# Kernel tuning notes

Hardware: AMD Instinct MI355X
Metric: run time of the kernel (lower is better)

The kernel has to match this reference:

```python
import jax, jax.numpy as jnp
import numpy as np

NB_OBJECTS = 3
DIM_BODY = 10
DIM_OBJECT = 15
DIM_OBJ_FEAT = NB_OBJECTS + DIM_OBJECT  # 18
DIM_PHI_IN = 54
HID = 256
DIM_PHI_OUT = 256
DIM_RHO_OUT = 1
B = 65536

# (o1, o2) object pair and (j, k) predicate indices, as in the torch code
PAIRS = [((0, 1), (3, 5)), ((0, 2), (4, 7)), ((1, 2), (6, 8))]


def setup_inputs() -> dict:
    key = jax.random.key(0)
    ks = jax.random.split(key, 24)
    inp = {
        "obs": jax.random.normal(ks[0], (B, 55), dtype=jnp.float32),
        "ag": jax.random.uniform(ks[1], (B, 9), dtype=jnp.float32),
        "g": jax.random.uniform(ks[2], (B, 9), dtype=jnp.float32),
        "anchor_g": jax.random.uniform(ks[3], (B, 9), dtype=jnp.float32),
        "act": jax.random.normal(ks[4], (B, 4), dtype=jnp.float32),
    }
    s = 0.05
    # PhiCriticDeepSet: two independent 2-layer MLPs (streams 1 and 2)
    inp["w1"] = jax.random.normal(ks[5], (DIM_PHI_IN, HID), dtype=jnp.float32) * s
    inp["b1"] = jnp.zeros((HID,), dtype=jnp.float32)
    inp["w2"] = jax.random.normal(ks[6], (HID, DIM_PHI_OUT), dtype=jnp.float32) * s
    inp["b2"] = jnp.zeros((DIM_PHI_OUT,), dtype=jnp.float32)
    inp["w3"] = jax.random.normal(ks[7], (DIM_PHI_IN, HID), dtype=jnp.float32) * s
    inp["b3"] = jnp.zeros((HID,), dtype=jnp.float32)
    inp["w4"] = jax.random.normal(ks[8], (HID, DIM_PHI_OUT), dtype=jnp.float32) * s
    inp["b4"] = jnp.zeros((DIM_PHI_OUT,), dtype=jnp.float32)
    # RhoCriticDeepSet: two independent 2-layer heads
    inp["w5"] = jax.random.normal(ks[9], (DIM_PHI_OUT, HID), dtype=jnp.float32) * s
    inp["b5"] = jnp.zeros((HID,), dtype=jnp.float32)
    inp["w6"] = jax.random.normal(ks[10], (HID, DIM_RHO_OUT), dtype=jnp.float32) * s
    inp["b6"] = jnp.zeros((DIM_RHO_OUT,), dtype=jnp.float32)
    inp["w7"] = jax.random.normal(ks[11], (DIM_PHI_OUT, HID), dtype=jnp.float32) * s
    inp["b7"] = jnp.zeros((HID,), dtype=jnp.float32)
    inp["w8"] = jax.random.normal(ks[12], (HID, DIM_RHO_OUT), dtype=jnp.float32) * s
    inp["b8"] = jnp.zeros((DIM_RHO_OUT,), dtype=jnp.float32)
    return inp


def _build_pair_inputs(obs, ag, g, act, anchor_g):
    """combinations_trick branch: data-dependent gather of goal bits and object pairs."""
    bs = obs.shape[0]
    obs_body = obs[:, :DIM_BODY]
    eye = jnp.eye(NB_OBJECTS, dtype=obs.dtype)
    # obs_objects: [3, B, 18] = one-hot(3) ++ object state(15)
    obs_objects = jnp.stack([
        jnp.concatenate([jnp.broadcast_to(eye[i], (bs, NB_OBJECTS)),
                         obs[:, DIM_BODY + DIM_OBJECT * i: DIM_BODY + DIM_OBJECT * (i + 1)]],
                        axis=1)
        for i in range(NB_OBJECTS)], axis=0)
    bidx = jnp.arange(bs)
    inputs = []
    for i, ((o1, o2), (j, k)) in enumerate(PAIRS):
        # selector = anchor_g @ [e_j, e_k] difference = anchor_g[:, j] - anchor_g[:, k]
        sel = (anchor_g[:, j] - anchor_g[:, k]) >= 0  # [B] bool
        # idxs_bits[i] = [i, j] where sel else [i, k]
        bit2 = jnp.where(sel, j, k)  # [B] int
        ag_pair = jnp.stack([ag[:, i], ag[bidx, bit2]], axis=1)  # [B, 2]
        g_pair = jnp.stack([g[:, i], g[bidx, bit2]], axis=1)     # [B, 2]
        # idxs_objects[i] = [o1, o2] where sel else [o2, o1]
        oi = jnp.where(sel, o1, o2)  # [B]
        oj = jnp.where(sel, o2, o1)
        obj_first = obs_objects[oi, bidx]   # [B, 18] gather along object axis
        obj_second = obs_objects[oj, bidx]  # [B, 18]
        inputs.append(jnp.concatenate(
            [ag_pair, g_pair, obs_body, obj_first, obj_second, act], axis=1))
    return jnp.stack(inputs)  # [3, B, 54]


def reference(obs, ag, g, anchor_g, act,
              w1, b1, w2, b2, w3, b3, w4, b4,
              w5, b5, w6, b6, w7, b7, w8, b8):
    inp = _build_pair_inputs(obs, ag, g, act, anchor_g)  # [3, B, 54]
    # PhiCriticDeepSet (two relu-relu streams)
    x1 = jax.nn.relu(jnp.einsum('pbi,ih->pbh', jax.nn.relu(jnp.einsum('pbd,dh->pbh', inp, w1) + b1), w2) + b2)
    x2 = jax.nn.relu(jnp.einsum('pbi,ih->pbh', jax.nn.relu(jnp.einsum('pbd,dh->pbh', inp, w3) + b3), w4) + b4)
    s1 = x1.sum(axis=0)  # [B, 256] deepset sum over pairs
    s2 = x2.sum(axis=0)
    # RhoCriticDeepSet readouts
    q1 = jax.nn.relu(s1 @ w5 + b5) @ w6 + b6  # [B, 1]
    q2 = jax.nn.relu(s2 @ w7 + b7) @ w8 + b8  # [B, 1]
    return (q1, q2)
```

## Files before the change

### kernel.cpp

```cpp
#include <hip/hip_runtime.h>
#include <hip/hip_bf16.h>

typedef unsigned short u16;
typedef unsigned int   u32;

using bf8 = __attribute__((ext_vector_type(8))) __bf16;
using f4  = __attribute__((ext_vector_type(4))) float;

__device__ __forceinline__ float b2f(u16 u) {
    union { u32 i; float f; } v; v.i = ((u32)u) << 16; return v.f;
}
__device__ __forceinline__ u16 f2b(float f) {
    union { float f; u32 i; } v; v.f = f;
    u32 x = v.i;
    x += 0x7fffu + ((x >> 16) & 1u);
    return (u16)(x >> 16);
}
__device__ __forceinline__ u32 pk2(float lo, float hi) {
    union { __hip_bfloat162 h; u32 u; } v;
    v.h = __float22bfloat162_rn(make_float2(lo, hi));
    return v.u;
}

__global__ void swz_all(const float* __restrict__ w1, const float* __restrict__ w3,
                        const float* __restrict__ w2, const float* __restrict__ w4,
                        const float* __restrict__ w5, const float* __restrict__ w7,
                        u16* __restrict__ ws) {
    __shared__ u16 slab[32 * 270];
    int b = blockIdx.x, t = threadIdx.x;
    const float* src; u16* dst; int kmax, kt;
    if      (b <  2) { src = w1; dst = ws;          kmax = 54;  kt = b;      }
    else if (b <  4) { src = w3; dst = ws + 16384;  kmax = 54;  kt = b - 2;  }
    else if (b < 12) { src = w2; dst = ws + 32768;  kmax = 256; kt = b - 4;  }
    else if (b < 20) { src = w4; dst = ws + 98304;  kmax = 256; kt = b - 12; }
    else if (b < 28) { src = w5; dst = ws + 163840; kmax = 256; kt = b - 20; }
    else             { src = w7; dst = ws + 229376; kmax = 256; kt = b - 28; }

    #pragma unroll
    for (int it = 0; it < 8; ++it) {
        int flat = it * 1024 + t * 4;
        int row = flat >> 8, col = flat & 255;
        int k = kt * 32 + row;
        float4 v = make_float4(0.f, 0.f, 0.f, 0.f);
        if (k < kmax) v = *(const float4*)(src + k * 256 + col);
        u32* sp = (u32*)&slab[row * 270 + col];
        sp[0] = pk2(v.x, v.y);
        sp[1] = pk2(v.z, v.w);
    }
    __syncthreads();

    int lane = t & 63, wave = t >> 6, lr = lane & 15, kg = lane >> 4;
    #pragma unroll
    for (int i = 0; i < 4; ++i) {
        int ct = wave * 4 + i;
        u16 v[8];
        #pragma unroll
        for (int j = 0; j < 8; ++j)
            v[j] = slab[(kg * 8 + j) * 270 + ct * 16 + lr];
        uint4 o;
        o.x = (u32)v[0] | ((u32)v[1] << 16);
        o.y = (u32)v[2] | ((u32)v[3] << 16);
        o.z = (u32)v[4] | ((u32)v[5] << 16);
        o.w = (u32)v[6] | ((u32)v[7] << 16);
        *(uint4*)(dst + (size_t)(((kt * 16 + ct) * 64 + lane) * 8)) = o;
    }
}

#define H_OFF 6144
#define S2O   (32 * 256)
#define RH0O  (64 * 256)

__global__ __launch_bounds__(512, 4) void critic_kernel(
    const float* __restrict__ obs, const float* __restrict__ ag,
    const float* __restrict__ g,   const float* __restrict__ anchor,
    const float* __restrict__ act,
    const float* __restrict__ b1,  const float* __restrict__ b2,
    const float* __restrict__ b3,  const float* __restrict__ b4,
    const float* __restrict__ b5,  const float* __restrict__ b7,
    const float* __restrict__ w6,  const float* __restrict__ b6,
    const float* __restrict__ w8,  const float* __restrict__ b8,
    const u16* __restrict__ wsz, float* __restrict__ out, int B) {

    __shared__ u16 pool[H_OFF + 96 * 256];

    const int t    = threadIdx.x;
    const int lane = t & 63;
    const int wave = t >> 6;
    const int lr   = lane & 15;
    const int lg   = lane >> 4;
    const int wg   = blockIdx.x;
    const int swr  = (lr & 7) << 3;

    if (t < 192) {
        const int O1[3] = {0, 0, 1}, O2[3] = {1, 2, 2};
        const int JA[3] = {3, 4, 6}, KA[3] = {5, 7, 8};
        int rr = t >> 1, part = t & 1;
        int p = rr >> 5, bl = rr & 31;
        int b = wg * 32 + bl;
        int j = JA[p], k = KA[p];
        bool sel = (anchor[b * 9 + j] - anchor[b * 9 + k]) >= 0.0f;
        u16* row = &pool[rr * 64];
        const int sw = (rr & 7) << 3;
        const u16 ONE = 0x3F80;
        if (part == 0) {
            int bit2 = sel ? j : k;
            int oi = sel ? O1[p] : O2[p];
            row[0 ^ sw] = f2b(ag[b * 9 + p]);
            row[1 ^ sw] = f2b(ag[b * 9 + bit2]);
            row[2 ^ sw] = f2b(g[b * 9 + p]);
            row[3 ^ sw] = f2b(g[b * 9 + bit2]);
            for (int c = 0; c < 10; ++c) row[(4 + c) ^ sw] = f2b(obs[b * 55 + c]);
            row[14 ^ sw] = (oi == 0) ? ONE : 0;
            row[15 ^ sw] = (oi == 1) ? ONE : 0;
            row[16 ^ sw] = (oi == 2) ? ONE : 0;
            for (int c = 0; c < 15; ++c) row[(17 + c) ^ sw] = f2b(obs[b * 55 + 10 + 15 * oi + c]);
        } else {
            int oj = sel ? O2[p] : O1[p];
            row[32 ^ sw] = (oj == 0) ? ONE : 0;
            row[33 ^ sw] = (oj == 1) ? ONE : 0;
            row[34 ^ sw] = (oj == 2) ? ONE : 0;
            for (int c = 0; c < 15; ++c) row[(35 + c) ^ sw] = f2b(obs[b * 55 + 10 + 15 * oj + c]);
            for (int c = 0; c < 4; ++c)  row[(50 + c) ^ sw] = f2b(act[b * 4 + c]);
            for (int c = 54; c < 64; ++c) row[c ^ sw] = 0;
        }
    }
    __syncthreads();

    u32 s1w[2][2][2];
    u32 s2w[2][2][2];

    for (int net = 0; net < 2; ++net) {
        const u16* Wl1 = wsz + (net ? 16384 : 0);
        const u16* Wl2 = wsz + 32768 + (net ? 65536 : 0);
        const float* bl1 = net ? b3 : b1;
        const float* bl2 = net ? b4 : b2;

        f4 acc[6][2];
        #pragma unroll
        for (int rt = 0; rt < 6; ++rt)
            #pragma unroll
            for (int c = 0; c < 2; ++c) acc[rt][c] = (f4){0.f, 0.f, 0.f, 0.f};
        __builtin_amdgcn_s_setprio(1);
        #pragma unroll
        for (int kt = 0; kt < 2; ++kt) {
            bf8 wfr[2];
            #pragma unroll
            for (int c = 0; c < 2; ++c)
                wfr[c] = *(const bf8*)(Wl1 + (size_t)(((kt * 16 + wave * 2 + c) * 64 + lane) * 8));
            #pragma unroll
            for (int rt = 0; rt < 6; ++rt) {
                bf8 xfr = *(const bf8*)(&pool[(rt * 16 + lr) * 64 + ((kt * 32 + lg * 8) ^ swr)]);
                #pragma unroll
                for (int c = 0; c < 2; ++c)
                    acc[rt][c] = __builtin_amdgcn_mfma_f32_16x16x32_bf16(wfr[c], xfr, acc[rt][c], 0, 0, 0);
            }
        }
        __builtin_amdgcn_s_setprio(0);
        #pragma unroll
        for (int c = 0; c < 2; ++c) {
            float4 bv = *(const float4*)(bl1 + (wave * 2 + c) * 16 + lg * 4);
            #pragma unroll
            for (int rt = 0; rt < 6; ++rt) {
                uint2 w;
                w.x = pk2(fmaxf(acc[rt][c][0] + bv.x, 0.f), fmaxf(acc[rt][c][1] + bv.y, 0.f));
                w.y = pk2(fmaxf(acc[rt][c][2] + bv.z, 0.f), fmaxf(acc[rt][c][3] + bv.w, 0.f));
                *(uint2*)&pool[H_OFF + (rt * 16 + lr) * 256 + ((((wave * 2 + c) * 16) + lg * 4) ^ swr)] = w;
            }
        }
        __syncthreads();

        f4 acc2[6][2];
        #pragma unroll
        for (int rt = 0; rt < 6; ++rt)
            #pragma unroll
            for (int c = 0; c < 2; ++c) acc2[rt][c] = (f4){0.f, 0.f, 0.f, 0.f};
        __builtin_amdgcn_s_setprio(1);
        #pragma unroll
        for (int ks = 0; ks < 8; ++ks) {
            bf8 wfr[2];
            #pragma unroll
            for (int c = 0; c < 2; ++c)
                wfr[c] = *(const bf8*)(Wl2 + (size_t)(((ks * 16 + wave * 2 + c) * 64 + lane) * 8));
            #pragma unroll
            for (int rt = 0; rt < 6; ++rt) {
                bf8 hfr = *(const bf8*)(&pool[H_OFF + (rt * 16 + lr) * 256 + ((ks * 32 + lg * 8) ^ swr)]);
                #pragma unroll
                for (int c = 0; c < 2; ++c)
                    acc2[rt][c] = __builtin_amdgcn_mfma_f32_16x16x32_bf16(wfr[c], hfr, acc2[rt][c], 0, 0, 0);
            }
        }
        __builtin_amdgcn_s_setprio(0);
        #pragma unroll
        for (int c = 0; c < 2; ++c) {
            float4 bv = *(const float4*)(bl2 + (wave * 2 + c) * 16 + lg * 4);
            #pragma unroll
            for (int s = 0; s < 2; ++s) {
                f4 sv = (f4){0.f, 0.f, 0.f, 0.f};
                #pragma unroll
                for (int p = 0; p < 3; ++p) {
                    sv[0] += fmaxf(acc2[p * 2 + s][c][0] + bv.x, 0.f);
                    sv[1] += fmaxf(acc2[p * 2 + s][c][1] + bv.y, 0.f);
                    sv[2] += fmaxf(acc2[p * 2 + s][c][2] + bv.z, 0.f);
                    sv[3] += fmaxf(acc2[p * 2 + s][c][3] + bv.w, 0.f);
                }
                if (net == 0) {
                    s1w[s][c][0] = pk2(sv[0], sv[1]);
                    s1w[s][c][1] = pk2(sv[2], sv[3]);
                } else {
                    s2w[s][c][0] = pk2(sv[0], sv[1]);
                    s2w[s][c][1] = pk2(sv[2], sv[3]);
                }
            }
        }
        __syncthreads();
    }

    #pragma unroll
    for (int s = 0; s < 2; ++s)
        #pragma unroll
        for (int c = 0; c < 2; ++c) {
            int base = H_OFF + (s * 16 + lr) * 256 + ((((wave * 2 + c) * 16) + lg * 4) ^ swr);
            *(uint2*)&pool[base]       = *(uint2*)&s1w[s][c][0];
            *(uint2*)&pool[base + S2O] = *(uint2*)&s2w[s][c][0];
        }
    __syncthreads();

    {
        const u16* W5 = wsz + 163840;
        const u16* W7 = wsz + 229376;
        f4 racc[4][2];
        #pragma unroll
        for (int rt = 0; rt < 4; ++rt)
            #pragma unroll
            for (int c = 0; c < 2; ++c) racc[rt][c] = (f4){0.f, 0.f, 0.f, 0.f};
        __builtin_amdgcn_s_setprio(1);
        #pragma unroll
        for (int ks = 0; ks < 8; ++ks) {
            bf8 w5f[2], w7f[2];
            #pragma unroll
            for (int c = 0; c < 2; ++c) {
                size_t off = (size_t)(((ks * 16 + wave * 2 + c) * 64 + lane) * 8);
                w5f[c] = *(const bf8*)(W5 + off);
                w7f[c] = *(const bf8*)(W7 + off);
            }
            #pragma unroll
            for (int rt = 0; rt < 2; ++rt) {
                bf8 s1f = *(const bf8*)(&pool[H_OFF + (rt * 16 + lr) * 256 + ((ks * 32 + lg * 8) ^ swr)]);
                bf8 s2f = *(const bf8*)(&pool[H_OFF + S2O + (rt * 16 + lr) * 256 + ((ks * 32 + lg * 8) ^ swr)]);
                #pragma unroll
                for (int c = 0; c < 2; ++c) {
                    racc[rt][c]     = __builtin_amdgcn_mfma_f32_16x16x32_bf16(w5f[c], s1f, racc[rt][c], 0, 0, 0);
                    racc[2 + rt][c] = __builtin_amdgcn_mfma_f32_16x16x32_bf16(w7f[c], s2f, racc[2 + rt][c], 0, 0, 0);
                }
            }
        }
        __builtin_amdgcn_s_setprio(0);
        #pragma unroll
        for (int c = 0; c < 2; ++c) {
            float4 bv = *(const float4*)(b5 + (wave * 2 + c) * 16 + lg * 4);
            #pragma unroll
            for (int rt = 0; rt < 2; ++rt) {
                uint2 w;
                w.x = pk2(fmaxf(racc[rt][c][0] + bv.x, 0.f), fmaxf(racc[rt][c][1] + bv.y, 0.f));
                w.y = pk2(fmaxf(racc[rt][c][2] + bv.z, 0.f), fmaxf(racc[rt][c][3] + bv.w, 0.f));
                *(uint2*)&pool[H_OFF + RH0O + (rt * 16 + lr) * 256 + ((((wave * 2 + c) * 16) + lg * 4) ^ swr)] = w;
            }
        }
        __syncthreads();
        #pragma unroll
        for (int c = 0; c < 2; ++c) {
            float4 bv = *(const float4*)(b7 + (wave * 2 + c) * 16 + lg * 4);
            #pragma unroll
            for (int rt = 0; rt < 2; ++rt) {
                uint2 w;
                w.x = pk2(fmaxf(racc[2 + rt][c][0] + bv.x, 0.f), fmaxf(racc[2 + rt][c][1] + bv.y, 0.f));
                w.y = pk2(fmaxf(racc[2 + rt][c][2] + bv.z, 0.f), fmaxf(racc[2 + rt][c][3] + bv.w, 0.f));
                *(uint2*)&pool[H_OFF + (rt * 16 + lr) * 256 + ((((wave * 2 + c) * 16) + lg * 4) ^ swr)] = w;
            }
        }
        __syncthreads();
    }

    {
        int net = lane >> 5, r = lane & 31;
        int hoff = net ? H_OFF : H_OFF + RH0O;
        const float* wv = net ? w8 : w6;
        const int swq = (r & 7) << 3;
        float s = 0.f;
        #pragma unroll
        for (int it = 0; it < 8; ++it) {
            uint2 two = *(const uint2*)&pool[hoff + r * 256 + ((wave * 32 + it * 4) ^ swq)];
            float4 wq = *(const float4*)(wv + wave * 32 + it * 4);
            s += __uint_as_float(two.x << 16)          * wq.x;
            s += __uint_as_float(two.x & 0xffff0000u)  * wq.y;
            s += __uint_as_float(two.y << 16)          * wq.z;
            s += __uint_as_float(two.y & 0xffff0000u)  * wq.w;
        }
        ((u32*)pool)[t] = __float_as_uint(s);
    }
    __syncthreads();
    if (t < 64) {
        int net = t >> 5, r = t & 31;
        float qv = net ? b8[0] : b6[0];
        #pragma unroll
        for (int p = 0; p < 8; ++p)
            qv += __uint_as_float(((u32*)pool)[p * 64 + t]);
        out[net * B + wg * 32 + r] = qv;
    }
}

extern "C" void kernel_launch(void* const* d_in, const int* in_sizes, int n_in,
                              void* d_out, int out_size, void* d_ws, size_t ws_size,
                              hipStream_t stream) {
    const float* obs = (const float*)d_in[0];
    const float* ag  = (const float*)d_in[1];
    const float* g   = (const float*)d_in[2];
    const float* anc = (const float*)d_in[3];
    const float* act = (const float*)d_in[4];
    const float* w1  = (const float*)d_in[5];
    const float* b1  = (const float*)d_in[6];
    const float* w2  = (const float*)d_in[7];
    const float* b2  = (const float*)d_in[8];
    const float* w3  = (const float*)d_in[9];
    const float* b3  = (const float*)d_in[10];
    const float* w4  = (const float*)d_in[11];
    const float* b4  = (const float*)d_in[12];
    const float* w5  = (const float*)d_in[13];
    const float* b5  = (const float*)d_in[14];
    const float* w6  = (const float*)d_in[15];
    const float* b6  = (const float*)d_in[16];
    const float* w7  = (const float*)d_in[17];
    const float* b7  = (const float*)d_in[18];
    const float* w8  = (const float*)d_in[19];
    const float* b8  = (const float*)d_in[20];
    u16* ws    = (u16*)d_ws;
    float* out = (float*)d_out;
    int B = in_sizes[0] / 55;

    swz_all<<<36, 256, 0, stream>>>(w1, w3, w2, w4, w5, w7, ws);
    critic_kernel<<<(B + 31) / 32, 512, 0, stream>>>(obs, ag, g, anc, act,
                                                     b1, b2, b3, b4, b5, b7,
                                                     w6, b6, w8, b8, ws, out, B);
}
```

Measured before the change: 191.4 us.

## Retile waves as 2x4 grid so each wave reuses X fragments across four column tiles

Changes the 8-wave work split from each wave owning 2 output-column tiles across all 6 row tiles to a 2x4 grid. Each wave now owns 4 column tiles and 3 row tiles (one per pair, for half the batch rows). The per-pair deepset sum stays within a wave, and in the rho stage each wave row handles one head (W5 or W7). This halves LDS activation-fragment reads per MFMA but doubles weight-fragment global loads per wave. Per-wave MFMA count and accumulator count are unchanged.

```diff
diff --git a/kernel.cpp b/kernel.cpp
--- a/kernel.cpp
+++ b/kernel.cpp
@@ -86,6 +86,8 @@
     const int t    = threadIdx.x;
     const int lane = t & 63;
     const int wave = t >> 6;
+    const int wr   = wave >> 2;
+    const int wc   = wave & 3;
     const int lr   = lane & 15;
     const int lg   = lane >> 4;
     const int wg   = blockIdx.x;
@@ -126,8 +128,8 @@
     }
     __syncthreads();
 
-    u32 s1w[2][2][2];
-    u32 s2w[2][2][2];
+    u32 s1w[4][2];
+    u32 s2w[4][2];
 
     for (int net = 0; net < 2; ++net) {
         const u16* Wl1 = wsz + (net ? 16384 : 0);
@@ -135,147 +137,140 @@
         const float* bl1 = net ? b3 : b1;
         const float* bl2 = net ? b4 : b2;
 
-        f4 acc[6][2];
-        #pragma unroll
-        for (int rt = 0; rt < 6; ++rt)
-            #pragma unroll
-            for (int c = 0; c < 2; ++c) acc[rt][c] = (f4){0.f, 0.f, 0.f, 0.f};
+        f4 acc[3][4];
+        #pragma unroll
+        for (int p = 0; p < 3; ++p)
+            #pragma unroll
+            for (int c = 0; c < 4; ++c) acc[p][c] = (f4){0.f, 0.f, 0.f, 0.f};
         __builtin_amdgcn_s_setprio(1);
         #pragma unroll
         for (int kt = 0; kt < 2; ++kt) {
-            bf8 wfr[2];
-            #pragma unroll
-            for (int c = 0; c < 2; ++c)
-                wfr[c] = *(const bf8*)(Wl1 + (size_t)(((kt * 16 + wave * 2 + c) * 64 + lane) * 8));
-            #pragma unroll
-            for (int rt = 0; rt < 6; ++rt) {
-                bf8 xfr = *(const bf8*)(&pool[(rt * 16 + lr) * 64 + ((kt * 32 + lg * 8) ^ swr)]);
-                #pragma unroll
-                for (int c = 0; c < 2; ++c)
-                    acc[rt][c] = __builtin_amdgcn_mfma_f32_16x16x32_bf16(wfr[c], xfr, acc[rt][c], 0, 0, 0);
+            bf8 wfr[4];
+            #pragma unroll
+            for (int c = 0; c < 4; ++c)
+                wfr[c] = *(const bf8*)(Wl1 + (size_t)(((kt * 16 + wc * 4 + c) * 64 + lane) * 8));
+            #pragma unroll
+            for (int p = 0; p < 3; ++p) {
+                bf8 xfr = *(const bf8*)(&pool[((2 * p + wr) * 16 + lr) * 64 + ((kt * 32 + lg * 8) ^ swr)]);
+                #pragma unroll
+                for (int c = 0; c < 4; ++c)
+                    acc[p][c] = __builtin_amdgcn_mfma_f32_16x16x32_bf16(wfr[c], xfr, acc[p][c], 0, 0, 0);
             }
         }
         __builtin_amdgcn_s_setprio(0);
         #pragma unroll
-        for (int c = 0; c < 2; ++c) {
-            float4 bv = *(const float4*)(bl1 + (wave * 2 + c) * 16 + lg * 4);
-            #pragma unroll
-            for (int rt = 0; rt < 6; ++rt) {
+        for (int c = 0; c < 4; ++c) {
+            float4 bv = *(const float4*)(bl1 + (wc * 4 + c) * 16 + lg * 4);
+            #pragma unroll
+            for (int p = 0; p < 3; ++p) {
                 uint2 w;
-                w.x = pk2(fmaxf(acc[rt][c][0] + bv.x, 0.f), fmaxf(acc[rt][c][1] + bv.y, 0.f));
-                w.y = pk2(fmaxf(acc[rt][c][2] + bv.z, 0.f), fmaxf(acc[rt][c][3] + bv.w, 0.f));
-                *(uint2*)&pool[H_OFF + (rt * 16 + lr) * 256 + ((((wave * 2 + c) * 16) + lg * 4) ^ swr)] = w;
+                w.x = pk2(fmaxf(acc[p][c][0] + bv.x, 0.f), fmaxf(acc[p][c][1] + bv.y, 0.f));
+                w.y = pk2(fmaxf(acc[p][c][2] + bv.z, 0.f), fmaxf(acc[p][c][3] + bv.w, 0.f));
+                *(uint2*)&pool[H_OFF + ((2 * p + wr) * 16 + lr) * 256 + ((((wc * 4 + c) * 16) + lg * 4) ^ swr)] = w;
             }
         }
         __syncthreads();
 
-        f4 acc2[6][2];
-        #pragma unroll
-        for (int rt = 0; rt < 6; ++rt)
-            #pragma unroll
-            for (int c = 0; c < 2; ++c) acc2[rt][c] = (f4){0.f, 0.f, 0.f, 0.f};
+        f4 acc2[3][4];
+        #pragma unroll
+        for (int p = 0; p < 3; ++p)
+            #pragma unroll
+            for (int c = 0; c < 4; ++c) acc2[p][c] = (f4){0.f, 0.f, 0.f, 0.f};
         __builtin_amdgcn_s_setprio(1);
         #pragma unroll
         for (int ks = 0; ks < 8; ++ks) {
-            bf8 wfr[2];
-            #pragma unroll
-            for (int c = 0; c < 2; ++c)
-                wfr[c] = *(const bf8*)(Wl2 + (size_t)(((ks * 16 + wave * 2 + c) * 64 + lane) * 8));
-            #pragma unroll
-            for (int rt = 0; rt < 6; ++rt) {
-                bf8 hfr = *(const bf8*)(&pool[H_OFF + (rt * 16 + lr) * 256 + ((ks * 32 + lg * 8) ^ swr)]);
-                #pragma unroll
-                for (int c = 0; c < 2; ++c)
-                    acc2[rt][c] = __builtin_amdgcn_mfma_f32_16x16x32_bf16(wfr[c], hfr, acc2[rt][c], 0, 0, 0);
+            bf8 wfr[4];
+            #pragma unroll
+            for (int c = 0; c < 4; ++c)
+                wfr[c] = *(const bf8*)(Wl2 + (size_t)(((ks * 16 + wc * 4 + c) * 64 + lane) * 8));
+            #pragma unroll
+            for (int p = 0; p < 3; ++p) {
+                bf8 hfr = *(const bf8*)(&pool[H_OFF + ((2 * p + wr) * 16 + lr) * 256 + ((ks * 32 + lg * 8) ^ swr)]);
+                #pragma unroll
+                for (int c = 0; c < 4; ++c)
+                    acc2[p][c] = __builtin_amdgcn_mfma_f32_16x16x32_bf16(wfr[c], hfr, acc2[p][c], 0, 0, 0);
             }
         }
         __builtin_amdgcn_s_setprio(0);
         #pragma unroll
-        for (int c = 0; c < 2; ++c) {
-            float4 bv = *(const float4*)(bl2 + (wave * 2 + c) * 16 + lg * 4);
-            #pragma unroll
-            for (int s = 0; s < 2; ++s) {
-                f4 sv = (f4){0.f, 0.f, 0.f, 0.f};
-                #pragma unroll
-                for (int p = 0; p < 3; ++p) {
-                    sv[0] += fmaxf(acc2[p * 2 + s][c][0] + bv.x, 0.f);
-                    sv[1] += fmaxf(acc2[p * 2 + s][c][1] + bv.y, 0.f);
-                    sv[2] += fmaxf(acc2[p * 2 + s][c][2] + bv.z, 0.f);
-                    sv[3] += fmaxf(acc2[p * 2 + s][c][3] + bv.w, 0.f);
+        for (int c = 0; c < 4; ++c) {
+            float4 bv = *(const float4*)(bl2 + (wc * 4 + c) * 16 + lg * 4);
+            f4 sv = (f4){0.f, 0.f, 0.f, 0.f};
+            #pragma unroll
+            for (int p = 0; p < 3; ++p) {
+                sv[0] += fmaxf(acc2[p][c][0] + bv.x, 0.f);
+                sv[1] += fmaxf(acc2[p][c][1] + bv.y, 0.f);
+                sv[2] += fmaxf(acc2[p][c][2] + bv.z, 0.f);
+                sv[3] += fmaxf(acc2[p][c][3] + bv.w, 0.f);
+            }
+            if (net == 0) {
+                s1w[c][0] = pk2(sv[0], sv[1]);
+                s1w[c][1] = pk2(sv[2], sv[3]);
+            } else {
+                s2w[c][0] = pk2(sv[0], sv[1]);
+                s2w[c][1] = pk2(sv[2], sv[3]);
+            }
+        }
+        __syncthreads();
+    }
+
+    #pragma unroll
+    for (int c = 0; c < 4; ++c) {
+        int base = H_OFF + (wr * 16 + lr) * 256 + ((((wc * 4 + c) * 16) + lg * 4) ^ swr);
+        *(uint2*)&pool[base]       = *(uint2*)&s1w[c][0];
+        *(uint2*)&pool[base + S2O] = *(uint2*)&s2w[c][0];
+    }
+    __syncthreads();
+
+    {
+        const u16* Wr  = wsz + (wr ? 229376 : 163840);
+        const int soff = wr ? S2O : 0;
+        f4 racc[2][4];
+        #pragma unroll
+        for (int rt = 0; rt < 2; ++rt)
+            #pragma unroll
+            for (int c = 0; c < 4; ++c) racc[rt][c] = (f4){0.f, 0.f, 0.f, 0.f};
+        __builtin_amdgcn_s_setprio(1);
+        #pragma unroll
+        for (int ks = 0; ks < 8; ++ks) {
+            bf8 wf[4];
+            #pragma unroll
+            for (int c = 0; c < 4; ++c)
+                wf[c] = *(const bf8*)(Wr + (size_t)(((ks * 16 + wc * 4 + c) * 64 + lane) * 8));
+            #pragma unroll
+            for (int rt = 0; rt < 2; ++rt) {
+                bf8 sf = *(const bf8*)(&pool[H_OFF + soff + (rt * 16 + lr) * 256 + ((ks * 32 + lg * 8) ^ swr)]);
+                #pragma unroll
+                for (int c = 0; c < 4; ++c)
+                    racc[rt][c] = __builtin_amdgcn_mfma_f32_16x16x32_bf16(wf[c], sf, racc[rt][c], 0, 0, 0);
+            }
+        }
+        __builtin_amdgcn_s_setprio(0);
+        if (wr == 0) {
+            #pragma unroll
+            for (int c = 0; c < 4; ++c) {
+                float4 bv = *(const float4*)(b5 + (wc * 4 + c) * 16 + lg * 4);
+                #pragma unroll
+                for (int rt = 0; rt < 2; ++rt) {
+                    uint2 w;
+                    w.x = pk2(fmaxf(racc[rt][c][0] + bv.x, 0.f), fmaxf(racc[rt][c][1] + bv.y, 0.f));
+                    w.y = pk2(fmaxf(racc[rt][c][2] + bv.z, 0.f), fmaxf(racc[rt][c][3] + bv.w, 0.f));
+                    *(uint2*)&pool[H_OFF + RH0O + (rt * 16 + lr) * 256 + ((((wc * 4 + c) * 16) + lg * 4) ^ swr)] = w;
                 }
-                if (net == 0) {
-                    s1w[s][c][0] = pk2(sv[0], sv[1]);
-                    s1w[s][c][1] = pk2(sv[2], sv[3]);
-                } else {
-                    s2w[s][c][0] = pk2(sv[0], sv[1]);
-                    s2w[s][c][1] = pk2(sv[2], sv[3]);
+            }
+        }
+        __syncthreads();
+        if (wr == 1) {
+            #pragma unroll
+            for (int c = 0; c < 4; ++c) {
+                float4 bv = *(const float4*)(b7 + (wc * 4 + c) * 16 + lg * 4);
+                #pragma unroll
+                for (int rt = 0; rt < 2; ++rt) {
+                    uint2 w;
+                    w.x = pk2(fmaxf(racc[rt][c][0] + bv.x, 0.f), fmaxf(racc[rt][c][1] + bv.y, 0.f));
+                    w.y = pk2(fmaxf(racc[rt][c][2] + bv.z, 0.f), fmaxf(racc[rt][c][3] + bv.w, 0.f));
+                    *(uint2*)&pool[H_OFF + (rt * 16 + lr) * 256 + ((((wc * 4 + c) * 16) + lg * 4) ^ swr)] = w;
                 }
-            }
-        }
-        __syncthreads();
-    }
-
-    #pragma unroll
-    for (int s = 0; s < 2; ++s)
-        #pragma unroll
-        for (int c = 0; c < 2; ++c) {
-            int base = H_OFF + (s * 16 + lr) * 256 + ((((wave * 2 + c) * 16) + lg * 4) ^ swr);
-            *(uint2*)&pool[base]       = *(uint2*)&s1w[s][c][0];
-            *(uint2*)&pool[base + S2O] = *(uint2*)&s2w[s][c][0];
-        }
-    __syncthreads();
-
-    {
-        const u16* W5 = wsz + 163840;
-        const u16* W7 = wsz + 229376;
-        f4 racc[4][2];
-        #pragma unroll
-        for (int rt = 0; rt < 4; ++rt)
-            #pragma unroll
-            for (int c = 0; c < 2; ++c) racc[rt][c] = (f4){0.f, 0.f, 0.f, 0.f};
-        __builtin_amdgcn_s_setprio(1);
-        #pragma unroll
-        for (int ks = 0; ks < 8; ++ks) {
-            bf8 w5f[2], w7f[2];
-            #pragma unroll
-            for (int c = 0; c < 2; ++c) {
-                size_t off = (size_t)(((ks * 16 + wave * 2 + c) * 64 + lane) * 8);
-                w5f[c] = *(const bf8*)(W5 + off);
-                w7f[c] = *(const bf8*)(W7 + off);
-            }
-            #pragma unroll
-            for (int rt = 0; rt < 2; ++rt) {
-                bf8 s1f = *(const bf8*)(&pool[H_OFF + (rt * 16 + lr) * 256 + ((ks * 32 + lg * 8) ^ swr)]);
-                bf8 s2f = *(const bf8*)(&pool[H_OFF + S2O + (rt * 16 + lr) * 256 + ((ks * 32 + lg * 8) ^ swr)]);
-                #pragma unroll
-                for (int c = 0; c < 2; ++c) {
-                    racc[rt][c]     = __builtin_amdgcn_mfma_f32_16x16x32_bf16(w5f[c], s1f, racc[rt][c], 0, 0, 0);
-                    racc[2 + rt][c] = __builtin_amdgcn_mfma_f32_16x16x32_bf16(w7f[c], s2f, racc[2 + rt][c], 0, 0, 0);
-                }
-            }
-        }
-        __builtin_amdgcn_s_setprio(0);
-        #pragma unroll
-        for (int c = 0; c < 2; ++c) {
-            float4 bv = *(const float4*)(b5 + (wave * 2 + c) * 16 + lg * 4);
-            #pragma unroll
-            for (int rt = 0; rt < 2; ++rt) {
-                uint2 w;
-                w.x = pk2(fmaxf(racc[rt][c][0] + bv.x, 0.f), fmaxf(racc[rt][c][1] + bv.y, 0.f));
-                w.y = pk2(fmaxf(racc[rt][c][2] + bv.z, 0.f), fmaxf(racc[rt][c][3] + bv.w, 0.f));
-                *(uint2*)&pool[H_OFF + RH0O + (rt * 16 + lr) * 256 + ((((wave * 2 + c) * 16) + lg * 4) ^ swr)] = w;
-            }
-        }
-        __syncthreads();
-        #pragma unroll
-        for (int c = 0; c < 2; ++c) {
-            float4 bv = *(const float4*)(b7 + (wave * 2 + c) * 16 + lg * 4);
-            #pragma unroll
-            for (int rt = 0; rt < 2; ++rt) {
-                uint2 w;
-                w.x = pk2(fmaxf(racc[2 + rt][c][0] + bv.x, 0.f), fmaxf(racc[2 + rt][c][1] + bv.y, 0.f));
-                w.y = pk2(fmaxf(racc[2 + rt][c][2] + bv.z, 0.f), fmaxf(racc[2 + rt][c][3] + bv.w, 0.f));
-                *(uint2*)&pool[H_OFF + (rt * 16 + lr) * 256 + ((((wave * 2 + c) * 16) + lg * 4) ^ swr)] = w;
             }
         }
         __syncthreads();
```

Result: slower. 377.1 us (+97.0%).
